# Kernel tuning notes

Measured on AMD Instinct MI355X. Metric: run time of the kernel, lower is better.

Reference implementation:

```python
import jax, jax.numpy as jnp
import numpy as np

N_NODES = 100000
N_EDGES = 600000
F_IN, HID, CLS = 128, 128, 16


def sage_conv(x, src, dst, W_l, b_l, W_r, n_nodes):
    # mean aggregation of neighbor features: message x[src] scattered to dst
    msg = x[src]                                              # [E, F]
    agg = jax.ops.segment_sum(msg, dst, num_segments=n_nodes)  # [N, F]
    deg = jax.ops.segment_sum(jnp.ones((src.shape[0],), x.dtype), dst, num_segments=n_nodes)
    agg = agg / jnp.maximum(deg, 1.0)[:, None]
    # PyG SAGEConv: lin_l(agg) (with bias) + lin_r(x_root) (no bias)
    return agg @ W_l + b_l + x @ W_r


def setup_inputs() -> dict:
    key = jax.random.key(0)
    ks = jax.random.split(key, 6)
    x = jax.random.normal(ks[0], (N_NODES, F_IN), jnp.float32)
    edge_index = jax.random.randint(ks[1], (2, N_EDGES), 0, N_NODES, dtype=jnp.int64)
    s1 = 1.0 / np.sqrt(F_IN)
    s2 = 1.0 / np.sqrt(HID)
    return {
        "x": x,
        "edge_index": edge_index,
        "W1_l": jax.random.normal(ks[2], (F_IN, HID), jnp.float32) * s1,
        "b1": jnp.zeros((HID,), jnp.float32),
        "W1_r": jax.random.normal(ks[3], (F_IN, HID), jnp.float32) * s1,
        "W2_l": jax.random.normal(ks[4], (HID, CLS), jnp.float32) * s2,
        "b2": jnp.zeros((CLS,), jnp.float32),
        "W2_r": jax.random.normal(ks[5], (HID, CLS), jnp.float32) * s2,
    }


def reference(x, edge_index, W1_l, b1, W1_r, W2_l, b2, W2_r):
    n = x.shape[0]
    src, dst = edge_index[0], edge_index[1]
    h = sage_conv(x, src, dst, W1_l, b1, W1_r, n)
    h = jax.nn.relu(h)
    # F.dropout(training=self.training): identity in eval mode
    out = sage_conv(h, src, dst, W2_l, b2, W2_r, n)
    return jax.nn.log_softmax(out, axis=1)
```

## Files before the change

### kernel.cpp

```cpp
#include <hip/hip_runtime.h>
#include <cstdint>

#define N_NODES 100000
#define N_PAD 100096
#define N_EDGES 600000
#define F 128
#define CLS 16
#define CAP 32

typedef short bf16x8 __attribute__((ext_vector_type(8)));
typedef float f32x4 __attribute__((ext_vector_type(4)));

__device__ inline float bf2f(unsigned int lo16) { return __uint_as_float(lo16 << 16); }
__device__ inline unsigned short f2b(float f) {
    unsigned int u = __float_as_uint(f);
    return (unsigned short)((u + 0x7fffu + ((u >> 16) & 1u)) >> 16);
}

__global__ __launch_bounds__(256) void init_k(int* __restrict__ deg,
                                              const float* __restrict__ x,
                                              unsigned short* __restrict__ xb,
                                              const float* __restrict__ W1l,
                                              const float* __restrict__ W1r,
                                              const float* __restrict__ W2l,
                                              const float* __restrict__ W2r,
                                              unsigned short* __restrict__ w1t,
                                              unsigned short* __restrict__ w2t) {
    int b = blockIdx.x;
    if (b < 98) {
        int i = b * 1024 + threadIdx.x * 4;
#pragma unroll
        for (int k = 0; k < 4; k++)
            if (i + k < N_NODES) deg[i + k] = 0;
    } else if (b < 12598) {
        int i = (b - 98) * 256 + threadIdx.x;
        if (i < N_NODES * F / 4) {
            float4 v = ((const float4*)x)[i];
            ushort4 o;
            o.x = f2b(v.x); o.y = f2b(v.y); o.z = f2b(v.z); o.w = f2b(v.w);
            ((ushort4*)xb)[i] = o;
        }
    } else if (b < 12726) {
        int idx = (b - 12598) * 256 + threadIdx.x;
        int n = idx >> 8, k = idx & 255;
        float v = (k < F) ? W1l[k * F + n] : W1r[(k - F) * F + n];
        int ct = n >> 4, m = n & 15;
        int half = k >> 7, ks = (k >> 5) & 3, quad = (k >> 3) & 3, j = k & 7;
        w1t[(ct * 8 + ks * 2 + half) * 512 + (quad * 16 + m) * 8 + j] = f2b(v);
    } else {
        int idx = (b - 12726) * 256 + threadIdx.x;
        if (idx < 32 * F) {
            int n = idx >> 7, k = idx & 127;
            float v = (n < CLS) ? W2l[k * CLS + n] : W2r[k * CLS + (n - CLS)];
            int tile = n >> 4, m = n & 15;
            int ks = (k >> 5) & 3, quad = (k >> 3) & 3, j = k & 7;
            w2t[(tile * 4 + ks) * 512 + (quad * 16 + m) * 8 + j] = f2b(v);
        }
    }
}

__global__ void fill_k(const int* __restrict__ src, const int* __restrict__ dst,
                       int* __restrict__ deg, int* __restrict__ bucket) {
    int e = blockIdx.x * blockDim.x + threadIdx.x;
    if (e < N_EDGES) {
        int d = dst[e];
        int slot = atomicAdd(&deg[d], 1);
        if (slot < CAP) bucket[d * CAP + slot] = src[e];
    }
}

__global__ __launch_bounds__(256) void agg_b_k(const unsigned short* __restrict__ feat,
                                               const int* __restrict__ deg,
                                               const int* __restrict__ bucket,
                                               unsigned short* __restrict__ outagg) {
    int tid = threadIdx.x;
    int node = blockIdx.x * 16 + (tid >> 4);
    int f8 = (tid & 15) * 8;
    const int* bk = bucket + node * CAP;

    int d_raw = deg[node];
    int4 b0 = *(const int4*)(bk);
    int4 b1 = *(const int4*)(bk + 4);
    int4 b2 = *(const int4*)(bk + 8);
    int n0  = min(max(b0.x, 0), N_NODES - 1);
    int n1  = min(max(b0.y, 0), N_NODES - 1);
    int n2  = min(max(b0.z, 0), N_NODES - 1);
    int n3  = min(max(b0.w, 0), N_NODES - 1);
    int n4  = min(max(b1.x, 0), N_NODES - 1);
    int n5  = min(max(b1.y, 0), N_NODES - 1);
    int n6  = min(max(b1.z, 0), N_NODES - 1);
    int n7  = min(max(b1.w, 0), N_NODES - 1);
    int n8  = min(max(b2.x, 0), N_NODES - 1);
    int n9  = min(max(b2.y, 0), N_NODES - 1);
    int n10 = min(max(b2.z, 0), N_NODES - 1);
    int n11 = min(max(b2.w, 0), N_NODES - 1);
    uint4 v0  = *(const uint4*)(feat + (size_t)n0 * F + f8);
    uint4 v1  = *(const uint4*)(feat + (size_t)n1 * F + f8);
    uint4 v2  = *(const uint4*)(feat + (size_t)n2 * F + f8);
    uint4 v3  = *(const uint4*)(feat + (size_t)n3 * F + f8);
    uint4 v4  = *(const uint4*)(feat + (size_t)n4 * F + f8);
    uint4 v5  = *(const uint4*)(feat + (size_t)n5 * F + f8);
    uint4 v6  = *(const uint4*)(feat + (size_t)n6 * F + f8);
    uint4 v7  = *(const uint4*)(feat + (size_t)n7 * F + f8);
    uint4 v8  = *(const uint4*)(feat + (size_t)n8 * F + f8);
    uint4 v9  = *(const uint4*)(feat + (size_t)n9 * F + f8);
    uint4 v10 = *(const uint4*)(feat + (size_t)n10 * F + f8);
    uint4 v11 = *(const uint4*)(feat + (size_t)n11 * F + f8);

    int d = min(d_raw, CAP);
    float acc[8] = {0.f, 0.f, 0.f, 0.f, 0.f, 0.f, 0.f, 0.f};
#define ACC8(vv) { \
    acc[0] += bf2f((vv).x & 0xffffu); acc[1] += bf2f((vv).x >> 16); \
    acc[2] += bf2f((vv).y & 0xffffu); acc[3] += bf2f((vv).y >> 16); \
    acc[4] += bf2f((vv).z & 0xffffu); acc[5] += bf2f((vv).z >> 16); \
    acc[6] += bf2f((vv).w & 0xffffu); acc[7] += bf2f((vv).w >> 16); }
    if (d > 0)  ACC8(v0);
    if (d > 1)  ACC8(v1);
    if (d > 2)  ACC8(v2);
    if (d > 3)  ACC8(v3);
    if (d > 4)  ACC8(v4);
    if (d > 5)  ACC8(v5);
    if (d > 6)  ACC8(v6);
    if (d > 7)  ACC8(v7);
    if (d > 8)  ACC8(v8);
    if (d > 9)  ACC8(v9);
    if (d > 10) ACC8(v10);
    if (d > 11) ACC8(v11);
    for (int j0 = 12; j0 < d; j0 += 4) {
        int4 bb = *(const int4*)(bk + j0);
        int m0 = min(max(bb.x, 0), N_NODES - 1);
        int m1 = min(max(bb.y, 0), N_NODES - 1);
        int m2 = min(max(bb.z, 0), N_NODES - 1);
        int m3 = min(max(bb.w, 0), N_NODES - 1);
        uint4 w0 = *(const uint4*)(feat + (size_t)m0 * F + f8);
        uint4 w1 = *(const uint4*)(feat + (size_t)m1 * F + f8);
        uint4 w2 = *(const uint4*)(feat + (size_t)m2 * F + f8);
        uint4 w3 = *(const uint4*)(feat + (size_t)m3 * F + f8);
        int rem = d - j0;
        if (rem > 0) ACC8(w0);
        if (rem > 1) ACC8(w1);
        if (rem > 2) ACC8(w2);
        if (rem > 3) ACC8(w3);
    }
#undef ACC8
    float inv = 1.0f / fmaxf((float)d, 1.0f);
    uint4 o;
    o.x = (unsigned int)f2b(acc[0] * inv) | ((unsigned int)f2b(acc[1] * inv) << 16);
    o.y = (unsigned int)f2b(acc[2] * inv) | ((unsigned int)f2b(acc[3] * inv) << 16);
    o.z = (unsigned int)f2b(acc[4] * inv) | ((unsigned int)f2b(acc[5] * inv) << 16);
    o.w = (unsigned int)f2b(acc[6] * inv) | ((unsigned int)f2b(acc[7] * inv) << 16);
    *(uint4*)(outagg + (size_t)node * F + f8) = o;
}

__global__ __launch_bounds__(256) void gemm_fused(const unsigned short* __restrict__ Ab,
                                                  const unsigned short* __restrict__ Xb,
                                                  const unsigned short* __restrict__ Wt,
                                                  const float* __restrict__ bias,
                                                  const unsigned short* __restrict__ Wt2,
                                                  unsigned short* __restrict__ trLb,
                                                  float* __restrict__ trR) {
    __shared__ unsigned short sh[128 * 132];
    int tid = threadIdx.x;
    int wave = tid >> 6, lane = tid & 63;
    int row0 = blockIdx.x * 128 + wave * 32;
    int m = lane & 15, quad = lane >> 4;
    int koff = quad * 8;

    const unsigned short* pa0 = Ab + (size_t)(row0 + m) * F + koff;
    const unsigned short* pa1 = pa0 + 16 * F;
    const unsigned short* px0 = Xb + (size_t)(row0 + m) * F + koff;
    const unsigned short* px1 = px0 + 16 * F;
    const unsigned short* pw = Wt + lane * 8;

    f32x4 acc0[8], acc1[8];
#pragma unroll
    for (int ct = 0; ct < 8; ct++) { acc0[ct] = (f32x4){0,0,0,0}; acc1[ct] = (f32x4){0,0,0,0}; }

#pragma unroll
    for (int ks = 0; ks < 4; ks++) {
        bf16x8 a0 = *(const bf16x8*)(const void*)(pa0 + ks * 32);
        bf16x8 a1 = *(const bf16x8*)(const void*)(pa1 + ks * 32);
        bf16x8 x0 = *(const bf16x8*)(const void*)(px0 + ks * 32);
        bf16x8 x1 = *(const bf16x8*)(const void*)(px1 + ks * 32);
#pragma unroll
        for (int ct = 0; ct < 8; ct++) {
            bf16x8 bl = *(const bf16x8*)(const void*)(pw + (ct * 8 + ks * 2 + 0) * 512);
            bf16x8 br = *(const bf16x8*)(const void*)(pw + (ct * 8 + ks * 2 + 1) * 512);
            acc0[ct] = __builtin_amdgcn_mfma_f32_16x16x32_bf16(a0, bl, acc0[ct], 0, 0, 0);
            acc1[ct] = __builtin_amdgcn_mfma_f32_16x16x32_bf16(a1, bl, acc1[ct], 0, 0, 0);
            acc0[ct] = __builtin_amdgcn_mfma_f32_16x16x32_bf16(x0, br, acc0[ct], 0, 0, 0);
            acc1[ct] = __builtin_amdgcn_mfma_f32_16x16x32_bf16(x1, br, acc1[ct], 0, 0, 0);
        }
    }

    int lr0 = wave * 32 + quad * 4;
#pragma unroll
    for (int ct = 0; ct < 8; ct++) {
        int n = ct * 16 + m;
        float bv = bias[n];
#pragma unroll
        for (int r = 0; r < 4; r++) {
            sh[(lr0 + r) * 132 + n]      = f2b(fmaxf(acc0[ct][r] + bv, 0.f));
            sh[(lr0 + 16 + r) * 132 + n] = f2b(fmaxf(acc1[ct][r] + bv, 0.f));
        }
    }
    __syncthreads();

    const unsigned short* hl0 = sh + (wave * 32 + m) * 132 + koff;
    const unsigned short* hl1 = sh + (wave * 32 + 16 + m) * 132 + koff;
    const unsigned short* pw2 = Wt2 + lane * 8;

    f32x4 al0 = (f32x4){0,0,0,0}, al1 = (f32x4){0,0,0,0};
    f32x4 ar0 = (f32x4){0,0,0,0}, ar1 = (f32x4){0,0,0,0};
#pragma unroll
    for (int ks = 0; ks < 4; ks++) {
        bf16x8 h0 = *(const bf16x8*)(const void*)(hl0 + ks * 32);
        bf16x8 h1 = *(const bf16x8*)(const void*)(hl1 + ks * 32);
        bf16x8 wl = *(const bf16x8*)(const void*)(pw2 + (0 * 4 + ks) * 512);
        bf16x8 wr = *(const bf16x8*)(const void*)(pw2 + (1 * 4 + ks) * 512);
        al0 = __builtin_amdgcn_mfma_f32_16x16x32_bf16(h0, wl, al0, 0, 0, 0);
        al1 = __builtin_amdgcn_mfma_f32_16x16x32_bf16(h1, wl, al1, 0, 0, 0);
        ar0 = __builtin_amdgcn_mfma_f32_16x16x32_bf16(h0, wr, ar0, 0, 0, 0);
        ar1 = __builtin_amdgcn_mfma_f32_16x16x32_bf16(h1, wr, ar1, 0, 0, 0);
    }
    int r0 = row0 + quad * 4;
#pragma unroll
    for (int r = 0; r < 4; r++) {
        trLb[(size_t)(r0 + r) * CLS + m]      = f2b(al0[r]);
        trLb[(size_t)(r0 + 16 + r) * CLS + m] = f2b(al1[r]);
        trR[(size_t)(r0 + r) * CLS + m]       = ar0[r];
        trR[(size_t)(r0 + 16 + r) * CLS + m]  = ar1[r];
    }
}

__global__ __launch_bounds__(256) void agg2sm_k(const unsigned short* __restrict__ trLb,
                                                const float* __restrict__ trR,
                                                const int* __restrict__ deg,
                                                const int* __restrict__ bucket,
                                                const float* __restrict__ b2,
                                                float* __restrict__ out) {
    int node = blockIdx.x * 4 + (threadIdx.x >> 6);
    int lane = threadIdx.x & 63;
    int r = lane >> 2;
    int cq = (lane & 3) * 4;
    const int* bk = bucket + node * CAP;

    int d_raw = deg[node];
    int nb = min(max(bk[r], 0), N_NODES - 1);
    uint2 v = *(const uint2*)(trLb + (size_t)nb * CLS + cq);
    float4 selfR = *(const float4*)(trR + (size_t)node * CLS + cq);

    int d = min(d_raw, CAP);
    float4 acc = {0.f, 0.f, 0.f, 0.f};
    if (r < d) {
        acc.x += bf2f(v.x & 0xffffu); acc.y += bf2f(v.x >> 16);
        acc.z += bf2f(v.y & 0xffffu); acc.w += bf2f(v.y >> 16);
    }
    if (d > 16) {
        int idx = 16 + r;
        bool valid = idx < d;
        int m2 = bk[valid ? idx : 0];
        uint2 w = *(const uint2*)(trLb + (size_t)m2 * CLS + cq);
        if (valid) {
            acc.x += bf2f(w.x & 0xffffu); acc.y += bf2f(w.x >> 16);
            acc.z += bf2f(w.y & 0xffffu); acc.w += bf2f(w.y >> 16);
        }
    }
#pragma unroll
    for (int off = 4; off <= 32; off <<= 1) {
        acc.x += __shfl_xor(acc.x, off);
        acc.y += __shfl_xor(acc.y, off);
        acc.z += __shfl_xor(acc.z, off);
        acc.w += __shfl_xor(acc.w, off);
    }
    float inv = 1.0f / fmaxf((float)d, 1.0f);
    float4 bb = *(const float4*)(b2 + cq);
    float vx = acc.x * inv + selfR.x + bb.x;
    float vy = acc.y * inv + selfR.y + bb.y;
    float vz = acc.z * inv + selfR.z + bb.z;
    float vw = acc.w * inv + selfR.w + bb.w;
    float mx = fmaxf(fmaxf(vx, vy), fmaxf(vz, vw));
    mx = fmaxf(mx, __shfl_xor(mx, 1));
    mx = fmaxf(mx, __shfl_xor(mx, 2));
    float sm = __expf(vx - mx) + __expf(vy - mx) + __expf(vz - mx) + __expf(vw - mx);
    sm += __shfl_xor(sm, 1);
    sm += __shfl_xor(sm, 2);
    float lg = __logf(sm);
    if (r == 0) {
        float4 o = {vx - mx - lg, vy - mx - lg, vz - mx - lg, vw - mx - lg};
        *(float4*)(out + (size_t)node * CLS + cq) = o;
    }
}


extern "C" void kernel_launch(void* const* d_in, const int* in_sizes, int n_in,
                              void* d_out, int out_size, void* d_ws, size_t ws_size,
                              hipStream_t stream) {
    const float* x   = (const float*)d_in[0];
    const int*   ei  = (const int*)d_in[1];
    const float* W1l = (const float*)d_in[2];
    const float* b1  = (const float*)d_in[3];
    const float* W1r = (const float*)d_in[4];
    const float* W2l = (const float*)d_in[5];
    const float* b2  = (const float*)d_in[6];
    const float* W2r = (const float*)d_in[7];
    float* out = (float*)d_out;

    const int* src = ei;
    const int* dst = ei + N_EDGES;

    char* ws = (char*)d_ws;
    size_t off = 0;
    auto alloc = [&](size_t bytes) { char* p = ws + off; off += (bytes + 127) / 128 * 128; return p; };
    int* deg    = (int*)alloc((size_t)N_NODES * 4);
    int* bucket = (int*)alloc((size_t)N_NODES * CAP * 4);
    unsigned short* xb   = (unsigned short*)alloc((size_t)N_PAD * F * 2);
    unsigned short* aggb = (unsigned short*)alloc((size_t)N_PAD * F * 2);
    unsigned short* trLb = (unsigned short*)alloc((size_t)N_PAD * CLS * 2);
    float*          trR  = (float*)alloc((size_t)N_PAD * CLS * 4);
    unsigned short* w1t  = (unsigned short*)alloc((size_t)F * 256 * 2);
    unsigned short* w2t  = (unsigned short*)alloc((size_t)32 * F * 2);

    init_k<<<12743, 256, 0, stream>>>(deg, x, xb, W1l, W1r, W2l, W2r, w1t, w2t);
    fill_k<<<(N_EDGES + 255) / 256, 256, 0, stream>>>(src, dst, deg, bucket);
    agg_b_k<<<N_NODES / 16, 256, 0, stream>>>(xb, deg, bucket, aggb);
    gemm_fused<<<N_PAD / 128, 256, 0, stream>>>(aggb, xb, w1t, b1, w2t, trLb, trR);
    agg2sm_k<<<N_NODES / 4, 256, 0, stream>>>(trLb, trR, deg, bucket, b2, out);
}
```

Measured before the change: 218.7 us.

## Fuse layer-1 neighbor mean aggregation into the GEMM kernel via shared memory

Removes the separate aggregation kernel and computes each 128-row tile's neighbor means directly into shared memory before the MFMA GEMM. This eliminates the aggregated bf16 feature buffer's global write and re-read and one kernel launch. In exchange the gather now runs in far fewer blocks with a serial per-group loop over 8 nodes, reducing parallelism and latency hiding for the random gather. The shared tile row stride is padded to 136, and a barrier is added before reusing shared memory for the hidden activations.

```diff
diff --git a/kernel.cpp b/kernel.cpp
--- a/kernel.cpp
+++ b/kernel.cpp
@@ -69,106 +69,107 @@
     }
 }
 
-__global__ __launch_bounds__(256) void agg_b_k(const unsigned short* __restrict__ feat,
-                                               const int* __restrict__ deg,
-                                               const int* __restrict__ bucket,
-                                               unsigned short* __restrict__ outagg) {
-    int tid = threadIdx.x;
-    int node = blockIdx.x * 16 + (tid >> 4);
-    int f8 = (tid & 15) * 8;
-    const int* bk = bucket + node * CAP;
-
-    int d_raw = deg[node];
-    int4 b0 = *(const int4*)(bk);
-    int4 b1 = *(const int4*)(bk + 4);
-    int4 b2 = *(const int4*)(bk + 8);
-    int n0  = min(max(b0.x, 0), N_NODES - 1);
-    int n1  = min(max(b0.y, 0), N_NODES - 1);
-    int n2  = min(max(b0.z, 0), N_NODES - 1);
-    int n3  = min(max(b0.w, 0), N_NODES - 1);
-    int n4  = min(max(b1.x, 0), N_NODES - 1);
-    int n5  = min(max(b1.y, 0), N_NODES - 1);
-    int n6  = min(max(b1.z, 0), N_NODES - 1);
-    int n7  = min(max(b1.w, 0), N_NODES - 1);
-    int n8  = min(max(b2.x, 0), N_NODES - 1);
-    int n9  = min(max(b2.y, 0), N_NODES - 1);
-    int n10 = min(max(b2.z, 0), N_NODES - 1);
-    int n11 = min(max(b2.w, 0), N_NODES - 1);
-    uint4 v0  = *(const uint4*)(feat + (size_t)n0 * F + f8);
-    uint4 v1  = *(const uint4*)(feat + (size_t)n1 * F + f8);
-    uint4 v2  = *(const uint4*)(feat + (size_t)n2 * F + f8);
-    uint4 v3  = *(const uint4*)(feat + (size_t)n3 * F + f8);
-    uint4 v4  = *(const uint4*)(feat + (size_t)n4 * F + f8);
-    uint4 v5  = *(const uint4*)(feat + (size_t)n5 * F + f8);
-    uint4 v6  = *(const uint4*)(feat + (size_t)n6 * F + f8);
-    uint4 v7  = *(const uint4*)(feat + (size_t)n7 * F + f8);
-    uint4 v8  = *(const uint4*)(feat + (size_t)n8 * F + f8);
-    uint4 v9  = *(const uint4*)(feat + (size_t)n9 * F + f8);
-    uint4 v10 = *(const uint4*)(feat + (size_t)n10 * F + f8);
-    uint4 v11 = *(const uint4*)(feat + (size_t)n11 * F + f8);
-
-    int d = min(d_raw, CAP);
-    float acc[8] = {0.f, 0.f, 0.f, 0.f, 0.f, 0.f, 0.f, 0.f};
-#define ACC8(vv) { \
-    acc[0] += bf2f((vv).x & 0xffffu); acc[1] += bf2f((vv).x >> 16); \
-    acc[2] += bf2f((vv).y & 0xffffu); acc[3] += bf2f((vv).y >> 16); \
-    acc[4] += bf2f((vv).z & 0xffffu); acc[5] += bf2f((vv).z >> 16); \
-    acc[6] += bf2f((vv).w & 0xffffu); acc[7] += bf2f((vv).w >> 16); }
-    if (d > 0)  ACC8(v0);
-    if (d > 1)  ACC8(v1);
-    if (d > 2)  ACC8(v2);
-    if (d > 3)  ACC8(v3);
-    if (d > 4)  ACC8(v4);
-    if (d > 5)  ACC8(v5);
-    if (d > 6)  ACC8(v6);
-    if (d > 7)  ACC8(v7);
-    if (d > 8)  ACC8(v8);
-    if (d > 9)  ACC8(v9);
-    if (d > 10) ACC8(v10);
-    if (d > 11) ACC8(v11);
-    for (int j0 = 12; j0 < d; j0 += 4) {
-        int4 bb = *(const int4*)(bk + j0);
-        int m0 = min(max(bb.x, 0), N_NODES - 1);
-        int m1 = min(max(bb.y, 0), N_NODES - 1);
-        int m2 = min(max(bb.z, 0), N_NODES - 1);
-        int m3 = min(max(bb.w, 0), N_NODES - 1);
-        uint4 w0 = *(const uint4*)(feat + (size_t)m0 * F + f8);
-        uint4 w1 = *(const uint4*)(feat + (size_t)m1 * F + f8);
-        uint4 w2 = *(const uint4*)(feat + (size_t)m2 * F + f8);
-        uint4 w3 = *(const uint4*)(feat + (size_t)m3 * F + f8);
-        int rem = d - j0;
-        if (rem > 0) ACC8(w0);
-        if (rem > 1) ACC8(w1);
-        if (rem > 2) ACC8(w2);
-        if (rem > 3) ACC8(w3);
-    }
-#undef ACC8
-    float inv = 1.0f / fmaxf((float)d, 1.0f);
-    uint4 o;
-    o.x = (unsigned int)f2b(acc[0] * inv) | ((unsigned int)f2b(acc[1] * inv) << 16);
-    o.y = (unsigned int)f2b(acc[2] * inv) | ((unsigned int)f2b(acc[3] * inv) << 16);
-    o.z = (unsigned int)f2b(acc[4] * inv) | ((unsigned int)f2b(acc[5] * inv) << 16);
-    o.w = (unsigned int)f2b(acc[6] * inv) | ((unsigned int)f2b(acc[7] * inv) << 16);
-    *(uint4*)(outagg + (size_t)node * F + f8) = o;
-}
-
-__global__ __launch_bounds__(256) void gemm_fused(const unsigned short* __restrict__ Ab,
-                                                  const unsigned short* __restrict__ Xb,
+__global__ __launch_bounds__(256) void gemm_fused(const unsigned short* __restrict__ Xb,
+                                                  const int* __restrict__ deg,
+                                                  const int* __restrict__ bucket,
                                                   const unsigned short* __restrict__ Wt,
                                                   const float* __restrict__ bias,
                                                   const unsigned short* __restrict__ Wt2,
                                                   unsigned short* __restrict__ trLb,
                                                   float* __restrict__ trR) {
-    __shared__ unsigned short sh[128 * 132];
+    __shared__ unsigned short sh[128 * 136];
     int tid = threadIdx.x;
+    int row0 = blockIdx.x * 128;
+
+    int grp = tid >> 4, l16 = tid & 15, f8 = l16 * 8;
+#pragma unroll 1
+    for (int rr = 0; rr < 8; rr++) {
+        int lr = grp * 8 + rr;
+        int node = row0 + lr;
+        const int* bk = bucket + (size_t)node * CAP;
+        int d_raw = deg[node];
+        int4 b0 = *(const int4*)(bk);
+        int4 b1 = *(const int4*)(bk + 4);
+        int4 b2 = *(const int4*)(bk + 8);
+        int n0  = min(max(b0.x, 0), N_NODES - 1);
+        int n1  = min(max(b0.y, 0), N_NODES - 1);
+        int n2  = min(max(b0.z, 0), N_NODES - 1);
+        int n3  = min(max(b0.w, 0), N_NODES - 1);
+        int n4  = min(max(b1.x, 0), N_NODES - 1);
+        int n5  = min(max(b1.y, 0), N_NODES - 1);
+        int n6  = min(max(b1.z, 0), N_NODES - 1);
+        int n7  = min(max(b1.w, 0), N_NODES - 1);
+        int n8  = min(max(b2.x, 0), N_NODES - 1);
+        int n9  = min(max(b2.y, 0), N_NODES - 1);
+        int n10 = min(max(b2.z, 0), N_NODES - 1);
+        int n11 = min(max(b2.w, 0), N_NODES - 1);
+        uint4 v0  = *(const uint4*)(Xb + (size_t)n0 * F + f8);
+        uint4 v1  = *(const uint4*)(Xb + (size_t)n1 * F + f8);
+        uint4 v2  = *(const uint4*)(Xb + (size_t)n2 * F + f8);
+        uint4 v3  = *(const uint4*)(Xb + (size_t)n3 * F + f8);
+        uint4 v4  = *(const uint4*)(Xb + (size_t)n4 * F + f8);
+        uint4 v5  = *(const uint4*)(Xb + (size_t)n5 * F + f8);
+        uint4 v6  = *(const uint4*)(Xb + (size_t)n6 * F + f8);
+        uint4 v7  = *(const uint4*)(Xb + (size_t)n7 * F + f8);
+        uint4 v8  = *(const uint4*)(Xb + (size_t)n8 * F + f8);
+        uint4 v9  = *(const uint4*)(Xb + (size_t)n9 * F + f8);
+        uint4 v10 = *(const uint4*)(Xb + (size_t)n10 * F + f8);
+        uint4 v11 = *(const uint4*)(Xb + (size_t)n11 * F + f8);
+
+        int d = (node < N_NODES) ? min(max(d_raw, 0), CAP) : 0;
+        float acc[8] = {0.f, 0.f, 0.f, 0.f, 0.f, 0.f, 0.f, 0.f};
+#define ACC8(vv) { \
+        acc[0] += bf2f((vv).x & 0xffffu); acc[1] += bf2f((vv).x >> 16); \
+        acc[2] += bf2f((vv).y & 0xffffu); acc[3] += bf2f((vv).y >> 16); \
+        acc[4] += bf2f((vv).z & 0xffffu); acc[5] += bf2f((vv).z >> 16); \
+        acc[6] += bf2f((vv).w & 0xffffu); acc[7] += bf2f((vv).w >> 16); }
+        if (d > 0)  ACC8(v0);
+        if (d > 1)  ACC8(v1);
+        if (d > 2)  ACC8(v2);
+        if (d > 3)  ACC8(v3);
+        if (d > 4)  ACC8(v4);
+        if (d > 5)  ACC8(v5);
+        if (d > 6)  ACC8(v6);
+        if (d > 7)  ACC8(v7);
+        if (d > 8)  ACC8(v8);
+        if (d > 9)  ACC8(v9);
+        if (d > 10) ACC8(v10);
+        if (d > 11) ACC8(v11);
+        for (int j0 = 12; j0 < d; j0 += 4) {
+            int4 bb = *(const int4*)(bk + j0);
+            int m0 = min(max(bb.x, 0), N_NODES - 1);
+            int m1 = min(max(bb.y, 0), N_NODES - 1);
+            int m2 = min(max(bb.z, 0), N_NODES - 1);
+            int m3 = min(max(bb.w, 0), N_NODES - 1);
+            uint4 w0 = *(const uint4*)(Xb + (size_t)m0 * F + f8);
+            uint4 w1 = *(const uint4*)(Xb + (size_t)m1 * F + f8);
+            uint4 w2 = *(const uint4*)(Xb + (size_t)m2 * F + f8);
+            uint4 w3 = *(const uint4*)(Xb + (size_t)m3 * F + f8);
+            int rem = d - j0;
+            if (rem > 0) ACC8(w0);
+            if (rem > 1) ACC8(w1);
+            if (rem > 2) ACC8(w2);
+            if (rem > 3) ACC8(w3);
+        }
+#undef ACC8
+        float inv = 1.0f / fmaxf((float)d, 1.0f);
+        uint4 o;
+        o.x = (unsigned int)f2b(acc[0] * inv) | ((unsigned int)f2b(acc[1] * inv) << 16);
+        o.y = (unsigned int)f2b(acc[2] * inv) | ((unsigned int)f2b(acc[3] * inv) << 16);
+        o.z = (unsigned int)f2b(acc[4] * inv) | ((unsigned int)f2b(acc[5] * inv) << 16);
+        o.w = (unsigned int)f2b(acc[6] * inv) | ((unsigned int)f2b(acc[7] * inv) << 16);
+        *(uint4*)&sh[lr * 136 + f8] = o;
+    }
+    __syncthreads();
+
     int wave = tid >> 6, lane = tid & 63;
-    int row0 = blockIdx.x * 128 + wave * 32;
     int m = lane & 15, quad = lane >> 4;
     int koff = quad * 8;
-
-    const unsigned short* pa0 = Ab + (size_t)(row0 + m) * F + koff;
-    const unsigned short* pa1 = pa0 + 16 * F;
-    const unsigned short* px0 = Xb + (size_t)(row0 + m) * F + koff;
+    int wrow0 = row0 + wave * 32;
+
+    const unsigned short* sa0 = sh + (wave * 32 + m) * 136 + koff;
+    const unsigned short* sa1 = sa0 + 16 * 136;
+    const unsigned short* px0 = Xb + (size_t)(wrow0 + m) * F + koff;
     const unsigned short* px1 = px0 + 16 * F;
     const unsigned short* pw = Wt + lane * 8;
 
@@ -178,8 +179,8 @@
 
 #pragma unroll
     for (int ks = 0; ks < 4; ks++) {
-        bf16x8 a0 = *(const bf16x8*)(const void*)(pa0 + ks * 32);
-        bf16x8 a1 = *(const bf16x8*)(const void*)(pa1 + ks * 32);
+        bf16x8 a0 = *(const bf16x8*)(const void*)(sa0 + ks * 32);
+        bf16x8 a1 = *(const bf16x8*)(const void*)(sa1 + ks * 32);
         bf16x8 x0 = *(const bf16x8*)(const void*)(px0 + ks * 32);
         bf16x8 x1 = *(const bf16x8*)(const void*)(px1 + ks * 32);
 #pragma unroll
@@ -192,6 +193,7 @@
             acc1[ct] = __builtin_amdgcn_mfma_f32_16x16x32_bf16(x1, br, acc1[ct], 0, 0, 0);
         }
     }
+    __syncthreads();
 
     int lr0 = wave * 32 + quad * 4;
 #pragma unroll
@@ -200,14 +202,14 @@
         float bv = bias[n];
 #pragma unroll
         for (int r = 0; r < 4; r++) {
-            sh[(lr0 + r) * 132 + n]      = f2b(fmaxf(acc0[ct][r] + bv, 0.f));
-            sh[(lr0 + 16 + r) * 132 + n] = f2b(fmaxf(acc1[ct][r] + bv, 0.f));
+            sh[(lr0 + r) * 136 + n]      = f2b(fmaxf(acc0[ct][r] + bv, 0.f));
+            sh[(lr0 + 16 + r) * 136 + n] = f2b(fmaxf(acc1[ct][r] + bv, 0.f));
         }
     }
     __syncthreads();
 
-    const unsigned short* hl0 = sh + (wave * 32 + m) * 132 + koff;
-    const unsigned short* hl1 = sh + (wave * 32 + 16 + m) * 132 + koff;
+    const unsigned short* hl0 = sh + (wave * 32 + m) * 136 + koff;
+    const unsigned short* hl1 = hl0 + 16 * 136;
     const unsigned short* pw2 = Wt2 + lane * 8;
 
     f32x4 al0 = (f32x4){0,0,0,0}, al1 = (f32x4){0,0,0,0};
@@ -223,7 +225,7 @@
         ar0 = __builtin_amdgcn_mfma_f32_16x16x32_bf16(h0, wr, ar0, 0, 0, 0);
         ar1 = __builtin_amdgcn_mfma_f32_16x16x32_bf16(h1, wr, ar1, 0, 0, 0);
     }
-    int r0 = row0 + quad * 4;
+    int r0 = wrow0 + quad * 4;
 #pragma unroll
     for (int r = 0; r < 4; r++) {
         trLb[(size_t)(r0 + r) * CLS + m]      = f2b(al0[r]);
@@ -315,7 +317,6 @@
     int* deg    = (int*)alloc((size_t)N_NODES * 4);
     int* bucket = (int*)alloc((size_t)N_NODES * CAP * 4);
     unsigned short* xb   = (unsigned short*)alloc((size_t)N_PAD * F * 2);
-    unsigned short* aggb = (unsigned short*)alloc((size_t)N_PAD * F * 2);
     unsigned short* trLb = (unsigned short*)alloc((size_t)N_PAD * CLS * 2);
     float*          trR  = (float*)alloc((size_t)N_PAD * CLS * 4);
     unsigned short* w1t  = (unsigned short*)alloc((size_t)F * 256 * 2);
@@ -323,7 +324,6 @@
 
     init_k<<<12743, 256, 0, stream>>>(deg, x, xb, W1l, W1r, W2l, W2r, w1t, w2t);
     fill_k<<<(N_EDGES + 255) / 256, 256, 0, stream>>>(src, dst, deg, bucket);
-    agg_b_k<<<N_NODES / 16, 256, 0, stream>>>(xb, deg, bucket, aggb);
-    gemm_fused<<<N_PAD / 128, 256, 0, stream>>>(aggb, xb, w1t, b1, w2t, trLb, trR);
+    gemm_fused<<<N_PAD / 128, 256, 0, stream>>>(xb, deg, bucket, w1t, b1, w2t, trLb, trR);
     agg2sm_k<<<N_NODES / 4, 256, 0, stream>>>(trLb, trR, deg, bucket, b2, out);
 }
```

Result: no change. 219.7 us (+0.5%).
